# Optimization experiments

Hardware: AMD Instinct MI355X
Metric: run time of the kernel (lower is better)

The kernel has to match this reference:

```python
import jax, jax.numpy as jnp
import numpy as np

N_EMBD = 512
HEAD_SIZE = 64
T = 4096
B = 4


def setup_inputs() -> dict:
    key = jax.random.key(0)
    kx, kq, kk, kv = jax.random.split(key, 4)
    x = jax.random.normal(kx, (B, T, N_EMBD), dtype=jnp.float32)
    # torch nn.Linear(n_embd, head_size, bias=False): weight [head_size, n_embd];
    # stored here transposed as [n_embd, head_size] so projection is x @ W.
    s = 1.0 / np.sqrt(N_EMBD)
    Wq = jax.random.uniform(kq, (N_EMBD, HEAD_SIZE), jnp.float32, -s, s)
    Wk = jax.random.uniform(kk, (N_EMBD, HEAD_SIZE), jnp.float32, -s, s)
    Wv = jax.random.uniform(kv, (N_EMBD, HEAD_SIZE), jnp.float32, -s, s)
    return {"x": x, "Wq": Wq, "Wk": Wk, "Wv": Wv}


def reference(x, Wq, Wk, Wv):
    Bq, Tq, C = x.shape
    q = x @ Wq  # [B,T,H]
    k = x @ Wk  # [B,T,H]
    v = x @ Wv  # [B,T,H]
    # NOTE: original scales by C**-0.5 with C = n_embd (input dim), not head_size.
    wei = jnp.einsum('bqh,bkh->bqk', q, k) * (C ** -0.5)  # [B,T,T]
    causal = jnp.tril(jnp.ones((Tq, Tq), dtype=bool))
    wei = jnp.where(causal, wei, -jnp.inf)
    wei = jax.nn.softmax(wei, axis=-1)
    # dropout p=0.0 -> identity (eval-mode deterministic baseline)
    out = jnp.einsum('bqk,bkh->bqh', wei, v)  # [B,T,H]
    return out
```

## Files before the change

kernel.cpp:

```cpp
#include <hip/hip_runtime.h>
#include <hip/hip_bf16.h>
#include <math.h>

#define T_SEQ 4096
#define NBATCH 4
#define C_EMB 512
#define HEAD 64
#define CHUNK 8
#define EPB 288

typedef __attribute__((ext_vector_type(8))) short short8;
typedef __attribute__((ext_vector_type(4))) short short4v;
typedef __attribute__((ext_vector_type(4))) float f32x4;

#define C2 (0.044194173824159216f * 1.44269504088896340736f)

__device__ __forceinline__ unsigned short f2bf(float f) {
    union { float f; unsigned u; } v; v.f = f;
    unsigned u = v.u;
    u += 0x7FFF + ((u >> 16) & 1);
    return (unsigned short)(u >> 16);
}
__device__ __forceinline__ unsigned pk2bf(float a, float b) {
    __hip_bfloat162 h = __float22bfloat162_rn(make_float2(a, b));
    return *(unsigned*)&h;
}
__device__ __forceinline__ float bf2f(unsigned short u) {
    union { unsigned u; float f; } v; v.u = ((unsigned)u) << 16;
    return v.f;
}

__global__ __launch_bounds__(64) void wcvt_kernel(
    const float* __restrict__ Wq, const float* __restrict__ Wk,
    const float* __restrict__ Wv, unsigned short* __restrict__ wt)
{
    const int w = blockIdx.x >> 6;
    const int n = blockIdx.x & 63;
    const float* W = (w == 0) ? Wq : (w == 1) ? Wk : Wv;
    const int k0 = threadIdx.x * 8;
    unsigned short tmp[8];
#pragma unroll
    for (int i = 0; i < 8; ++i) tmp[i] = f2bf(W[(size_t)(k0 + i) * HEAD + n]);
    *(short8*)(wt + ((size_t)blockIdx.x) * C_EMB + k0) = *(short8*)tmp;
}

__device__ __forceinline__ void ld_stage(const float* xp, int s, float4* xr) {
#pragma unroll
    for (int j = 0; j < 4; ++j) {
        xr[2 * j]     = *(const float4*)(xp + (s * 4 + j) * 32);
        xr[2 * j + 1] = *(const float4*)(xp + (s * 4 + j) * 32 + 4);
    }
}

__device__ __forceinline__ void mm_stage(const float4* xr, int s, int l16, int quad,
                                         int gbase,
                                         const unsigned short* __restrict__ wt,
                                         f32x4 acc[6]) {
#pragma unroll
    for (int j = 0; j < 4; ++j) {
        const int kc = s * 4 + j;
        float4 a = xr[2 * j], b = xr[2 * j + 1];
        int4 ai = make_int4((int)pk2bf(a.x, a.y), (int)pk2bf(a.z, a.w),
                            (int)pk2bf(b.x, b.y), (int)pk2bf(b.z, b.w));
        short8 af = *(short8*)&ai;
#pragma unroll
        for (int t = 0; t < 6; ++t) {
            short8 bf = *(const short8*)(wt + ((size_t)((gbase + t) * 16 + l16)) * C_EMB
                                            + kc * 32 + quad * 8);
            acc[t] = __builtin_amdgcn_mfma_f32_16x16x32_bf16(af, bf, acc[t], 0, 0, 0);
        }
    }
}

__global__ __launch_bounds__(256, 2) void proj_kernel(
    const float* __restrict__ x,
    const unsigned short* __restrict__ wt,
    unsigned short* __restrict__ qout,
    unsigned short* __restrict__ kout,
    unsigned short* __restrict__ vt)
{
    __shared__ unsigned short Vsh[64][40];

    const int tid    = threadIdx.x;
    const int wave   = tid >> 6;
    const int lane   = tid & 63;
    const int l16    = lane & 15;
    const int quad   = lane >> 4;
    const int rowblk = wave & 1;
    const int wgroup = wave >> 1;
    const int gbase  = wgroup * 6;
    const int row0   = blockIdx.x * 32;
    const int rowW   = row0 + rowblk * 16 + l16;

    f32x4 acc[6];
#pragma unroll
    for (int t = 0; t < 6; ++t) acc[t] = (f32x4){0.f, 0.f, 0.f, 0.f};

    const float* xp = x + (size_t)rowW * C_EMB + quad * 8;
    float4 xr[2][8];
    ld_stage(xp, 0, xr[0]);
#pragma unroll
    for (int s = 0; s < 4; ++s) {
        if (s < 3) ld_stage(xp, s + 1, xr[(s + 1) & 1]);
        mm_stage(xr[s & 1], s, l16, quad, gbase, wt, acc);
    }

#pragma unroll
    for (int r = 0; r < 4; ++r) {
        const int row = row0 + rowblk * 16 + quad * 4 + r;
        if (wgroup == 0) {
#pragma unroll
            for (int j = 0; j < 4; ++j)
                qout[(size_t)row * HEAD + j * 16 + l16] = f2bf(acc[j][r] * C2);
            kout[(size_t)row * HEAD + 0 * 16 + l16] = f2bf(acc[4][r]);
            kout[(size_t)row * HEAD + 1 * 16 + l16] = f2bf(acc[5][r]);
        } else {
            kout[(size_t)row * HEAD + 2 * 16 + l16] = f2bf(acc[0][r]);
            kout[(size_t)row * HEAD + 3 * 16 + l16] = f2bf(acc[1][r]);
#pragma unroll
            for (int j = 2; j < 6; ++j)
                Vsh[(j - 2) * 16 + l16][rowblk * 16 + quad * 4 + r] = f2bf(acc[j][r]);
        }
    }
    __syncthreads();
    {
        int h  = tid >> 2;
        int tc = (tid & 3) * 8;
        int b  = row0 >> 12;
        int t0 = row0 & (T_SEQ - 1);
        unsigned short* dst = vt + ((size_t)(b * HEAD + h)) * T_SEQ + t0 + tc;
        *(short8*)dst = *(const short8*)&Vsh[h][tc];
    }
}

__device__ __forceinline__ void stage_v(unsigned short (*Vbuf)[72], int sr, int phiA,
                                        short8 v0, short8 v1) {
    *(short4v*)&Vbuf[sr][phiA]      = __builtin_shufflevector(v0, v0, 0, 1, 2, 3);
    *(short4v*)&Vbuf[sr][phiA + 8]  = __builtin_shufflevector(v0, v0, 4, 5, 6, 7);
    *(short4v*)&Vbuf[sr][phiA + 16] = __builtin_shufflevector(v1, v1, 0, 1, 2, 3);
    *(short4v*)&Vbuf[sr][phiA + 24] = __builtin_shufflevector(v1, v1, 4, 5, 6, 7);
}

__global__ __launch_bounds__(256) void attn1_kernel(
    const unsigned short* __restrict__ qb,
    const unsigned short* __restrict__ kb,
    const unsigned short* __restrict__ vt,
    unsigned short* __restrict__ po,
    float* __restrict__ pl)
{
    __shared__ unsigned short Ks[2][64][72];
    __shared__ unsigned short Vs[2][64][72];

    const int tid  = threadIdx.x;
    const int wave = tid >> 6;
    const int lane = tid & 63;
    const int l16  = lane & 15;
    const int quad = lane >> 4;

    const int b = blockIdx.x / EPB;
    const int e = blockIdx.x % EPB;
    int g = 0;
#pragma unroll
    for (int gg = 1; gg < 8; ++gg) if (e >= 4 * gg * (gg + 1)) g = gg;
    const int rem = e - 4 * g * (g + 1);
    const int t   = rem / (g + 1);
    const int c   = rem - t * (g + 1);
    const int qt  = 8 * g + t;

    const size_t base = (size_t)b * T_SEQ;
    const int qrow = qt * 64 + wave * 16 + l16;
    short8 aq0 = *(const short8*)(qb + (base + qrow) * HEAD + quad * 8);
    short8 aq1 = *(const short8*)(qb + (base + qrow) * HEAD + 32 + quad * 8);

    float lacc = 0.f;
    f32x4 o[4];
#pragma unroll
    for (int n = 0; n < 4; ++n) o[n] = (f32x4){0.f, 0.f, 0.f, 0.f};

    const int kt0 = c * CHUNK;
    const int np  = min(CHUNK, qt + 1 - kt0);

    const int sr   = tid >> 2;
    const int sc   = (tid & 3) * 16;
    const int phiA = (sc & 32) + ((sc & 16) >> 2);

    short8 kra, krb, vra, vrb;
    {
        const int kbase = kt0 * 64;
        const unsigned short* ksrc = kb + (base + kbase + sr) * HEAD + sc;
        const unsigned short* vsrc = vt + ((size_t)(b * HEAD + sr)) * T_SEQ + kbase + sc;
        kra = *(const short8*)(ksrc);     krb = *(const short8*)(ksrc + 8);
        vra = *(const short8*)(vsrc);     vrb = *(const short8*)(vsrc + 8);
    }
    *(short8*)&Ks[0][sr][sc]     = kra;  *(short8*)&Ks[0][sr][sc + 8] = krb;
    stage_v(Vs[0], sr, phiA, vra, vrb);

    for (int p = 0; p < np; ++p) {
        const int cur = p & 1;
        const int kbase = (kt0 + p) * 64;
        __syncthreads();

        if (p + 1 < np) {
            const int nb = kbase + 64;
            const unsigned short* ksrc = kb + (base + nb + sr) * HEAD + sc;
            const unsigned short* vsrc = vt + ((size_t)(b * HEAD + sr)) * T_SEQ + nb + sc;
            kra = *(const short8*)(ksrc);  krb = *(const short8*)(ksrc + 8);
            vra = *(const short8*)(vsrc);  vrb = *(const short8*)(vsrc + 8);
        }

        f32x4 s[4];
#pragma unroll
        for (int n = 0; n < 4; ++n) {
            short8 bk0 = *(const short8*)&Ks[cur][n * 16 + l16][quad * 8];
            short8 bk1 = *(const short8*)&Ks[cur][n * 16 + l16][32 + quad * 8];
            f32x4 accS = (f32x4){0.f, 0.f, 0.f, 0.f};
            accS = __builtin_amdgcn_mfma_f32_16x16x32_bf16(bk0, aq0, accS, 0, 0, 0);
            accS = __builtin_amdgcn_mfma_f32_16x16x32_bf16(bk1, aq1, accS, 0, 0, 0);
            s[n] = accS;
        }

#pragma unroll
        for (int n = 0; n < 4; ++n)
#pragma unroll
            for (int r = 0; r < 4; ++r)
                s[n][r] = __builtin_amdgcn_exp2f(s[n][r]);

        if (kbase + 64 > qt * 64) {
            const int cb = kbase + quad * 4;
#pragma unroll
            for (int n = 0; n < 4; ++n)
#pragma unroll
                for (int r = 0; r < 4; ++r)
                    if (cb + n * 16 + r > qrow) s[n][r] = 0.f;
        }

#pragma unroll
        for (int n = 0; n < 4; ++n)
            lacc += (s[n][0] + s[n][1]) + (s[n][2] + s[n][3]);

#pragma unroll
        for (int st = 0; st < 2; ++st) {
            int4 ai = make_int4(
                (int)pk2bf(s[2 * st][0],     s[2 * st][1]),
                (int)pk2bf(s[2 * st][2],     s[2 * st][3]),
                (int)pk2bf(s[2 * st + 1][0], s[2 * st + 1][1]),
                (int)pk2bf(s[2 * st + 1][2], s[2 * st + 1][3]));
            short8 af = *(short8*)&ai;
#pragma unroll
            for (int n = 0; n < 4; ++n) {
                short8 bv = *(const short8*)&Vs[cur][n * 16 + l16][32 * st + quad * 8];
                o[n] = __builtin_amdgcn_mfma_f32_16x16x32_bf16(af, bv, o[n], 0, 0, 0);
            }
        }

        if (p + 1 < np) {
            const int nxt = cur ^ 1;
            *(short8*)&Ks[nxt][sr][sc]     = kra;  *(short8*)&Ks[nxt][sr][sc + 8] = krb;
            stage_v(Vs[nxt], sr, phiA, vra, vrb);
        }
    }

    lacc += __shfl_xor(lacc, 16);
    lacc += __shfl_xor(lacc, 32);

    const int pid = blockIdx.x;
#pragma unroll
    for (int n = 0; n < 4; ++n)
#pragma unroll
        for (int r = 0; r < 4; ++r) {
            int lr = wave * 16 + quad * 4 + r;
            po[(size_t)pid * 4096 + lr * 64 + n * 16 + l16] = f2bf(o[n][r]);
        }
    if (quad == 0)
        pl[pid * 64 + wave * 16 + l16] = lacc;
}

__global__ __launch_bounds__(256) void combine_kernel(
    const unsigned short* __restrict__ po, const float* __restrict__ pl,
    float* __restrict__ out)
{
    const int gth = blockIdx.x * 256 + threadIdx.x;
    const int h8  = gth & 7;
    const int row = gth >> 3;
    const int lr  = row & 63;
    const int qt  = (row >> 6) & 63;
    const int b   = row >> 12;
    const int nc  = (qt >> 3) + 1;
    const int g   = qt >> 3;
    const int rem = qt & 7;
    const int e0  = 4 * g * (g + 1) + rem * (g + 1);
    const int pid0 = b * EPB + e0;

    float l = 0.f;
    float acc[8];
#pragma unroll
    for (int i = 0; i < 8; ++i) acc[i] = 0.f;
    for (int cc = 0; cc < nc; ++cc) {
        l += pl[(pid0 + cc) * 64 + lr];
        short8 p8 = *(const short8*)(po + (size_t)(pid0 + cc) * 4096 + lr * 64 + h8 * 8);
#pragma unroll
        for (int i = 0; i < 8; ++i) acc[i] += bf2f((unsigned short)p8[i]);
    }
    float inv = 1.f / l;
    float4 r0 = make_float4(acc[0] * inv, acc[1] * inv, acc[2] * inv, acc[3] * inv);
    float4 r1 = make_float4(acc[4] * inv, acc[5] * inv, acc[6] * inv, acc[7] * inv);
    float* dst = out + (size_t)gth * 8;
    *(float4*)dst       = r0;
    *(float4*)(dst + 4) = r1;
}

extern "C" void kernel_launch(void* const* d_in, const int* in_sizes, int n_in,
                              void* d_out, int out_size, void* d_ws, size_t ws_size,
                              hipStream_t stream) {
    const float* x  = (const float*)d_in[0];
    const float* Wq = (const float*)d_in[1];
    const float* Wk = (const float*)d_in[2];
    const float* Wv = (const float*)d_in[3];
    float* out = (float*)d_out;

    char* ws = (char*)d_ws;
    unsigned short* qb = (unsigned short*)(ws);
    unsigned short* kb = (unsigned short*)(ws + (2u << 20));
    unsigned short* vt = (unsigned short*)(ws + (4u << 20));
    unsigned short* wt = (unsigned short*)(ws + (6u << 20));
    float* pl = (float*)(ws + (6u << 20) + 196608);
    unsigned short* po = (unsigned short*)(ws + (6u << 20) + 196608 + 294912);

    wcvt_kernel<<<dim3(192), dim3(64), 0, stream>>>(Wq, Wk, Wv, wt);
    proj_kernel<<<dim3(512), dim3(256), 0, stream>>>(x, wt, qb, kb, vt);
    attn1_kernel<<<dim3(NBATCH * EPB), dim3(256), 0, stream>>>(qb, kb, vt, po, pl);
    combine_kernel<<<dim3(512), dim3(256), 0, stream>>>(po, pl, out);
}
```

Measured before the change: 136.0 us.

## Split projection K dimension across waves with shared-memory reduction

The projection kernel used to split the 12 output column tiles (Q, K, V) between two wave groups, so each wave read the full 512-wide x row. Now each wave group covers half of the input dimension and all 12 tiles, and the partial sums are combined through shared memory before the write-out. This halves the x loads per wave and removes duplicated bf16 conversion of x. In exchange it doubles the accumulator registers (launch bounds drop the 2-blocks hint), adds a 24 KB shared reduction buffer and an extra barrier, and leaves half the waves idle during the epilogue.

```diff
diff --git a/kernel.cpp b/kernel.cpp
--- a/kernel.cpp
+++ b/kernel.cpp
@@ -52,33 +52,34 @@
     }
 }
 
-__device__ __forceinline__ void mm_stage(const float4* xr, int s, int l16, int quad,
-                                         int gbase,
+__device__ __forceinline__ void mm_stage(const float4* xr, int kb, int s,
+                                         int l16, int quad,
                                          const unsigned short* __restrict__ wt,
-                                         f32x4 acc[6]) {
+                                         f32x4 acc[12]) {
 #pragma unroll
     for (int j = 0; j < 4; ++j) {
-        const int kc = s * 4 + j;
+        const int kc = kb + s * 4 + j;
         float4 a = xr[2 * j], b = xr[2 * j + 1];
         int4 ai = make_int4((int)pk2bf(a.x, a.y), (int)pk2bf(a.z, a.w),
                             (int)pk2bf(b.x, b.y), (int)pk2bf(b.z, b.w));
         short8 af = *(short8*)&ai;
 #pragma unroll
-        for (int t = 0; t < 6; ++t) {
-            short8 bf = *(const short8*)(wt + ((size_t)((gbase + t) * 16 + l16)) * C_EMB
+        for (int t = 0; t < 12; ++t) {
+            short8 bf = *(const short8*)(wt + ((size_t)(t * 16 + l16)) * C_EMB
                                             + kc * 32 + quad * 8);
             acc[t] = __builtin_amdgcn_mfma_f32_16x16x32_bf16(af, bf, acc[t], 0, 0, 0);
         }
     }
 }
 
-__global__ __launch_bounds__(256, 2) void proj_kernel(
+__global__ __launch_bounds__(256) void proj_kernel(
     const float* __restrict__ x,
     const unsigned short* __restrict__ wt,
     unsigned short* __restrict__ qout,
     unsigned short* __restrict__ kout,
     unsigned short* __restrict__ vt)
 {
+    __shared__ f32x4 Red[2][12][64];
     __shared__ unsigned short Vsh[64][40];
 
     const int tid    = threadIdx.x;
@@ -87,40 +88,43 @@
     const int l16    = lane & 15;
     const int quad   = lane >> 4;
     const int rowblk = wave & 1;
-    const int wgroup = wave >> 1;
-    const int gbase  = wgroup * 6;
+    const int khalf  = wave >> 1;
     const int row0   = blockIdx.x * 32;
     const int rowW   = row0 + rowblk * 16 + l16;
 
-    f32x4 acc[6];
-#pragma unroll
-    for (int t = 0; t < 6; ++t) acc[t] = (f32x4){0.f, 0.f, 0.f, 0.f};
-
-    const float* xp = x + (size_t)rowW * C_EMB + quad * 8;
+    f32x4 acc[12];
+#pragma unroll
+    for (int t = 0; t < 12; ++t) acc[t] = (f32x4){0.f, 0.f, 0.f, 0.f};
+
+    const float* xp = x + (size_t)rowW * C_EMB + khalf * 256 + quad * 8;
+    const int kb = khalf * 8;
     float4 xr[2][8];
     ld_stage(xp, 0, xr[0]);
-#pragma unroll
-    for (int s = 0; s < 4; ++s) {
-        if (s < 3) ld_stage(xp, s + 1, xr[(s + 1) & 1]);
-        mm_stage(xr[s & 1], s, l16, quad, gbase, wt, acc);
-    }
-
-#pragma unroll
-    for (int r = 0; r < 4; ++r) {
-        const int row = row0 + rowblk * 16 + quad * 4 + r;
-        if (wgroup == 0) {
-#pragma unroll
-            for (int j = 0; j < 4; ++j)
-                qout[(size_t)row * HEAD + j * 16 + l16] = f2bf(acc[j][r] * C2);
-            kout[(size_t)row * HEAD + 0 * 16 + l16] = f2bf(acc[4][r]);
-            kout[(size_t)row * HEAD + 1 * 16 + l16] = f2bf(acc[5][r]);
-        } else {
-            kout[(size_t)row * HEAD + 2 * 16 + l16] = f2bf(acc[0][r]);
-            kout[(size_t)row * HEAD + 3 * 16 + l16] = f2bf(acc[1][r]);
-#pragma unroll
-            for (int j = 2; j < 6; ++j)
-                Vsh[(j - 2) * 16 + l16][rowblk * 16 + quad * 4 + r] = f2bf(acc[j][r]);
-        }
+    ld_stage(xp, 1, xr[1]);
+    mm_stage(xr[0], kb, 0, l16, quad, wt, acc);
+    mm_stage(xr[1], kb, 1, l16, quad, wt, acc);
+
+    if (khalf == 1) {
+#pragma unroll
+        for (int t = 0; t < 12; ++t) Red[rowblk][t][lane] = acc[t];
+    }
+    __syncthreads();
+    if (khalf == 0) {
+#pragma unroll
+        for (int t = 0; t < 12; ++t) {
+            f32x4 r = Red[rowblk][t][lane];
+#pragma unroll
+            for (int i = 0; i < 4; ++i) acc[t][i] += r[i];
+        }
+#pragma unroll
+        for (int n = 0; n < 4; ++n)
+#pragma unroll
+            for (int r = 0; r < 4; ++r) {
+                const int row = row0 + rowblk * 16 + quad * 4 + r;
+                qout[(size_t)row * HEAD + n * 16 + l16] = f2bf(acc[n][r] * C2);
+                kout[(size_t)row * HEAD + n * 16 + l16] = f2bf(acc[4 + n][r]);
+                Vsh[n * 16 + l16][rowblk * 16 + quad * 4 + r] = f2bf(acc[8 + n][r]);
+            }
     }
     __syncthreads();
     {
```

Result: no change. 133.7 us (-1.7%).
